# Kernel optimization log

Measured on AMD Instinct MI355X. Metric: run time of the kernel, lower is better.

Reference implementation:

```python
import jax, jax.numpy as jnp
import numpy as np

B, N, F_IN, H, F_OUT, NB = 4, 10000, 963, 128, 3, 3


def _gcn(x, adj, w, lw, b):
    # out = adj @ (x @ W) + x @ W_loop + bias   (adj shared across batch)
    return jnp.einsum('ij,bjf->bif', adj, x @ w) + x @ lw + b


def setup_inputs() -> dict:
    key = jax.random.key(0)
    ks = jax.random.split(key, 16)
    s = 0.02  # xavier-ish init scale
    adj = jax.random.uniform(ks[1], (N, N), dtype=jnp.float32) * (2.0 / N)  # normalized-adjacency surrogate
    return {
        'shape_verts': jax.random.normal(ks[0], (B, N, F_IN), dtype=jnp.float32),
        'adj': adj,
        'in_w': jax.random.normal(ks[2], (F_IN, H), dtype=jnp.float32) * s,
        'in_lw': jax.random.normal(ks[3], (F_IN, H), dtype=jnp.float32) * s,
        'in_b': jnp.zeros((H,), jnp.float32),
        'res_w1': jax.random.normal(ks[4], (NB, H, H), dtype=jnp.float32) * s,
        'res_lw1': jax.random.normal(ks[5], (NB, H, H), dtype=jnp.float32) * s,
        'res_b1': jnp.zeros((NB, H), jnp.float32),
        'res_w2': jax.random.normal(ks[6], (NB, H, H), dtype=jnp.float32) * s,
        'res_lw2': jax.random.normal(ks[7], (NB, H, H), dtype=jnp.float32) * s,
        'res_b2': jnp.zeros((NB, H), jnp.float32),
        'out_w': jax.random.normal(ks[8], (H, F_OUT), dtype=jnp.float32) * s,
        'out_lw': jax.random.normal(ks[9], (H, F_OUT), dtype=jnp.float32) * s,
        'out_b': jnp.zeros((F_OUT,), jnp.float32),
    }


def reference(shape_verts, adj, in_w, in_lw, in_b,
              res_w1, res_lw1, res_b1, res_w2, res_lw2, res_b2,
              out_w, out_lw, out_b):
    # GraphConvBottleneck.forward
    x = jax.nn.relu(_gcn(shape_verts, adj, in_w, in_lw, in_b))
    for i in range(NB):  # GraphConvResBlock
        h1 = jax.nn.relu(_gcn(x, adj, res_w1[i], res_lw1[i], res_b1[i]))
        h2 = jax.nn.relu(_gcn(h1, adj, res_w2[i], res_lw2[i], res_b2[i]))
        x = (x + h2) * 0.5
    x_out = _gcn(x, adj, out_w, out_lw, out_b)
    return (x_out, x)
```

## Files before the change

### kernel.cpp

```cpp
#include <hip/hip_runtime.h>
#include <stdint.h>

typedef unsigned short u16;
typedef __attribute__((ext_vector_type(8))) short short8;
typedef __attribute__((ext_vector_type(8))) unsigned short u16x8;
typedef __attribute__((ext_vector_type(4))) float f32x4;

#define NN    10000
#define NP    10016
#define MPADJ 10112
#define BB    4
#define HH    128
#define FIN   963
#define KIN   992
#define MR    40000
#define MRP   40064

__device__ __forceinline__ u16 f2bf(float f) {
  uint32_t u = __builtin_bit_cast(uint32_t, f);
  u += 0x7FFFu + ((u >> 16) & 1u);
  return (u16)(u >> 16);
}

__device__ __forceinline__ void gl2lds16(const void* g, void* l) {
  __builtin_amdgcn_global_load_lds((const __attribute__((address_space(1))) uint32_t*)g,
                                   (__attribute__((address_space(3))) uint32_t*)l, 16, 0, 0);
}


__global__ void conv_adj(const float* __restrict__ adj, u16* __restrict__ adjB) {
  int row = blockIdx.y;
  int j8 = blockIdx.x * 256 + threadIdx.x;
  if (j8 >= NP / 8) return;
  int j = j8 * 8;
  u16x8 o = {};
  if (row < NN && j < NN) {
    const float* p = adj + (size_t)row * NN + j;
    float4 a = *(const float4*)p;
    float4 b = *(const float4*)(p + 4);
    o[0] = f2bf(a.x); o[1] = f2bf(a.y); o[2] = f2bf(a.z); o[3] = f2bf(a.w);
    o[4] = f2bf(b.x); o[5] = f2bf(b.y); o[6] = f2bf(b.z); o[7] = f2bf(b.w);
  }
  *(u16x8*)(adjB + (size_t)row * NP + j) = o;
}

__global__ void conv_xin(const float* __restrict__ xin, u16* __restrict__ xinB) {
  int r = blockIdx.y;
  int f = blockIdx.x * 256 + threadIdx.x;
  if (f >= KIN) return;
  float v = 0.f;
  if (r < MR && f < FIN) v = xin[(size_t)r * FIN + f];
  xinB[(size_t)r * KIN + f] = f2bf(v);
}

__global__ void conv_w1(const float* __restrict__ wi, const float* __restrict__ lwi,
                        u16* __restrict__ Wt) {
  int tid = blockIdx.x * 256 + threadIdx.x;
  if (tid >= 256 * KIN) return;
  int c = tid / KIN, k = tid - c * KIN;
  float v = 0.f;
  if (k < FIN) v = (c < HH) ? wi[(size_t)k * HH + c] : lwi[(size_t)k * HH + (c - HH)];
  Wt[tid] = f2bf(v);
}

__global__ void conv_wres(const float* __restrict__ w1, const float* __restrict__ lw1,
                          const float* __restrict__ w2, const float* __restrict__ lw2,
                          u16* __restrict__ Wt) {
  int tid = blockIdx.x * 256 + threadIdx.x;
  if (tid >= 6 * 256 * HH) return;
  int l = tid / (256 * HH);
  int rem = tid - l * (256 * HH);
  int c = rem / HH, k = rem - c * HH;
  int blk = l >> 1;
  const float* W  = (l & 1) ? w2  : w1;
  const float* LW = (l & 1) ? lw2 : lw1;
  float v = (c < HH) ? W[((size_t)blk * HH + k) * HH + c]
                     : LW[((size_t)blk * HH + k) * HH + (c - HH)];
  Wt[tid] = f2bf(v);
}

__global__ void pad_zero(u16* tT, u16* xB, u16* h1B, u16* t3) {
  int tid = blockIdx.x * 256 + threadIdx.x;
  if (tid < 8192) {
    tT[(size_t)(tid >> 4) * NP + NN + (tid & 15)] = 0;
  } else if (tid < 16384) {
    xB[(size_t)MR * HH + (tid - 8192)] = 0;
  } else if (tid < 24576) {
    h1B[(size_t)MR * HH + (tid - 16384)] = 0;
  } else if (tid < 24832) {
    int t = tid - 24576;
    t3[(size_t)(t >> 4) * NP + NN + (t & 15)] = 0;
  }
}


__global__ __launch_bounds__(256) void gemm_big(const u16* __restrict__ A,
                                                const u16* __restrict__ Bt,
                                                float* __restrict__ P) {
  __shared__ u16 As[128 * 32];
  __shared__ u16 Bs[128 * 32];
  int mt_ = blockIdx.x, nt_ = blockIdx.y, s = blockIdx.z;
  int kt0 = (313 * s) / 3, kt1 = (313 * (s + 1)) / 3;
  int tid = threadIdx.x;
  int wave = tid >> 6, lane = tid & 63;
  int wm = wave >> 1, wn = wave & 1;
  int lr = lane >> 2, lc = (lane & 3) * 8;
  int ml = lane & 15, q = lane >> 4;

  const u16* Abase = A + (size_t)(mt_ * 128 + wave * 16 + lr) * NP + lc;
  const u16* Bbase = Bt + (size_t)(nt_ * 128 + wave * 16 + lr) * NP + lc;
  u16* lA = &As[(wave * 16) * 32];
  u16* lB = &Bs[(wave * 16) * 32];

  f32x4 acc[4][4] = {};
  for (int kt = kt0; kt < kt1; ++kt) {
    int k0 = kt * 32;
    __syncthreads();
    gl2lds16(Abase + k0, lA);
    gl2lds16(Abase + k0 + (size_t)64 * NP, lA + 64 * 32);
    gl2lds16(Bbase + k0, lB);
    gl2lds16(Bbase + k0 + (size_t)64 * NP, lB + 64 * 32);
    __syncthreads();
    short8 af[4], bf[4];
#pragma unroll
    for (int i = 0; i < 4; i++) af[i] = *(const short8*)&As[(wm * 64 + i * 16 + ml) * 32 + q * 8];
#pragma unroll
    for (int i = 0; i < 4; i++) bf[i] = *(const short8*)&Bs[(wn * 64 + i * 16 + ml) * 32 + q * 8];
#pragma unroll
    for (int i = 0; i < 4; i++)
#pragma unroll
      for (int j = 0; j < 4; j++)
        acc[i][j] = __builtin_amdgcn_mfma_f32_16x16x32_bf16(af[i], bf[j], acc[i][j], 0, 0, 0);
  }
  float* Ps = P + (size_t)s * NN * 512;
#pragma unroll
  for (int i = 0; i < 4; i++) {
    int row0 = mt_ * 128 + wm * 64 + i * 16 + q * 4;
#pragma unroll
    for (int j = 0; j < 4; j++) {
      int col = nt_ * 128 + wn * 64 + j * 16 + ml;
#pragma unroll
      for (int r = 0; r < 4; r++) {
        int row = row0 + r;
        if (row < NN) Ps[(size_t)row * 512 + col] = acc[i][j][r];
      }
    }
  }
}

__global__ __launch_bounds__(256) void gemm_small(const u16* __restrict__ A, int lda,
                                                  const u16* __restrict__ Wt, int ktiles,
                                                  const float* __restrict__ bias,
                                                  u16* __restrict__ tT, float* __restrict__ u) {
  __shared__ u16 As[128 * 32];
  __shared__ u16 Bs[128 * 32];
  int mt_ = blockIdx.x, half = blockIdx.y;
  int tid = threadIdx.x;
  int wave = tid >> 6, lane = tid & 63;
  int wm = wave >> 1, wn = wave & 1;
  int lr = lane >> 2, lc = (lane & 3) * 8;
  int ml = lane & 15, q = lane >> 4;

  const u16* Abase = A + (size_t)(mt_ * 128 + wave * 16 + lr) * lda + lc;
  const u16* Bbase = Wt + (size_t)(half * 128 + wave * 16 + lr) * lda + lc;
  u16* lA = &As[(wave * 16) * 32];
  u16* lB = &Bs[(wave * 16) * 32];

  f32x4 acc[4][4] = {};
  for (int kt = 0; kt < ktiles; ++kt) {
    int k0 = kt * 32;
    __syncthreads();
    gl2lds16(Abase + k0, lA);
    gl2lds16(Abase + k0 + (size_t)64 * lda, lA + 64 * 32);
    gl2lds16(Bbase + k0, lB);
    gl2lds16(Bbase + k0 + (size_t)64 * lda, lB + 64 * 32);
    __syncthreads();
    short8 af[4], bf[4];
#pragma unroll
    for (int i = 0; i < 4; i++) af[i] = *(const short8*)&As[(wm * 64 + i * 16 + ml) * 32 + q * 8];
#pragma unroll
    for (int i = 0; i < 4; i++) bf[i] = *(const short8*)&Bs[(wn * 64 + i * 16 + ml) * 32 + q * 8];
#pragma unroll
    for (int i = 0; i < 4; i++)
#pragma unroll
      for (int j = 0; j < 4; j++)
        acc[i][j] = __builtin_amdgcn_mfma_f32_16x16x32_bf16(af[i], bf[j], acc[i][j], 0, 0, 0);
  }
#pragma unroll
  for (int i = 0; i < 4; i++) {
    int row0 = mt_ * 128 + wm * 64 + i * 16 + q * 4;
#pragma unroll
    for (int j = 0; j < 4; j++) {
      int col = wn * 64 + j * 16 + ml;
#pragma unroll
      for (int r = 0; r < 4; r++) {
        int row = row0 + r;
        if (row < MR) {
          if (half == 0) {
            int b = row / NN;
            int n = row - b * NN;
            tT[(size_t)(b * 128 + col) * NP + n] = f2bf(acc[i][j][r]);
          } else {
            u[(size_t)row * HH + col] = acc[i][j][r] + bias[col];
          }
        }
      }
    }
  }
}

__global__ void reduce_act(const float* __restrict__ P, const float* __restrict__ u,
                           float* __restrict__ xf, u16* __restrict__ xB,
                           float* __restrict__ outx, int mode) {
  int tid = blockIdx.x * 256 + threadIdx.x;
  if (tid >= NN * 512) return;
  int n = tid >> 9, c = tid & 511;
  int b = c >> 7, h = c & 127;
  size_t uidx = (size_t)(b * NN + n) * HH + h;
  float v = P[tid] + P[5120000 + tid] + P[10240000 + tid] + u[uidx];
  v = v > 0.f ? v : 0.f;
  if (mode == 0) {
    xf[uidx] = v;
    xB[uidx] = f2bf(v);
  } else if (mode == 1) {
    xB[uidx] = f2bf(v);
  } else {
    float xn = (xf[uidx] + v) * 0.5f;
    xf[uidx] = xn;
    xB[uidx] = f2bf(xn);
    if (mode == 3) outx[uidx] = xn;
  }
}

__global__ void out_small(const float* __restrict__ x, const float* __restrict__ ow,
                          const float* __restrict__ olw, const float* __restrict__ ob,
                          u16* __restrict__ t3, float* __restrict__ u3) {
  int tid = blockIdx.x * 256 + threadIdx.x;
  if (tid >= NN * 16) return;
  int n = tid >> 4, c3 = tid & 15, b = c3 >> 2, f = c3 & 3;
  float tv = 0.f, uv = 0.f;
  if (f < 3) {
    const float* xr = x + (size_t)(b * NN + n) * HH;
    for (int k = 0; k < HH; k++) {
      float xv = xr[k];
      tv += xv * ow[k * 3 + f];
      uv += xv * olw[k * 3 + f];
    }
    uv += ob[f];
  }
  t3[(size_t)c3 * NP + n] = f2bf(tv);
  u3[tid] = uv;
}

__global__ __launch_bounds__(256) void gemm_skinny(const u16* __restrict__ A,
                                                   const u16* __restrict__ Bt,
                                                   float* __restrict__ P3) {
  __shared__ u16 As[64 * 32];
  __shared__ u16 Bs[16 * 32];
  int mt_ = blockIdx.x, s = blockIdx.y;
  int kt0 = (313 * s) / 2, kt1 = (313 * (s + 1)) / 2;
  int tid = threadIdx.x;
  int wave = tid >> 6, lane = tid & 63;
  int lr = lane >> 2, lc = (lane & 3) * 8;
  int ml = lane & 15, q = lane >> 4;

  const u16* Abase = A + (size_t)(mt_ * 64 + wave * 16 + lr) * NP + lc;
  const u16* Bbase = Bt + (size_t)lr * NP + lc;
  u16* lA = &As[(wave * 16) * 32];

  f32x4 acc = {};
  for (int kt = kt0; kt < kt1; ++kt) {
    int k0 = kt * 32;
    __syncthreads();
    gl2lds16(Abase + k0, lA);
    if (wave == 0) gl2lds16(Bbase + k0, &Bs[0]);
    __syncthreads();
    short8 af = *(const short8*)&As[(wave * 16 + ml) * 32 + q * 8];
    short8 bf = *(const short8*)&Bs[ml * 32 + q * 8];
    acc = __builtin_amdgcn_mfma_f32_16x16x32_bf16(af, bf, acc, 0, 0, 0);
  }
  float* Ps = P3 + (size_t)s * NP * 16;
  int row0 = mt_ * 64 + wave * 16 + q * 4;
#pragma unroll
  for (int r = 0; r < 4; r++) {
    int row = row0 + r;
    if (row < NN) Ps[(size_t)row * 16 + ml] = acc[r];
  }
}

__global__ void reduce3k(const float* __restrict__ P3, const float* __restrict__ u3,
                         float* __restrict__ out0) {
  int tid = blockIdx.x * 256 + threadIdx.x;
  if (tid >= NN * 12) return;
  int n = tid / 12;
  int rr = tid - n * 12;
  int b = rr / 3, f = rr - b * 3;
  int c3 = b * 4 + f;
  float v = P3[(size_t)n * 16 + c3] + P3[(size_t)NP * 16 + (size_t)n * 16 + c3] + u3[n * 16 + c3];
  out0[(size_t)(b * NN + n) * 3 + f] = v;
}


extern "C" void kernel_launch(void* const* d_in, const int* in_sizes, int n_in,
                              void* d_out, int out_size, void* d_ws, size_t ws_size,
                              hipStream_t stream) {
  (void)in_sizes; (void)n_in; (void)out_size; (void)ws_size;
  const float* xin    = (const float*)d_in[0];
  const float* adj    = (const float*)d_in[1];
  const float* in_w   = (const float*)d_in[2];
  const float* in_lw  = (const float*)d_in[3];
  const float* in_b   = (const float*)d_in[4];
  const float* res_w1 = (const float*)d_in[5];
  const float* res_lw1= (const float*)d_in[6];
  const float* res_b1 = (const float*)d_in[7];
  const float* res_w2 = (const float*)d_in[8];
  const float* res_lw2= (const float*)d_in[9];
  const float* res_b2 = (const float*)d_in[10];
  const float* out_w  = (const float*)d_in[11];
  const float* out_lw = (const float*)d_in[12];
  const float* out_b  = (const float*)d_in[13];

  char* wsp = (char*)d_ws;
  size_t off = 0;
  auto alloc = [&](size_t bytes) -> char* {
    char* p = wsp + off;
    off += (bytes + 255) & ~(size_t)255;
    return p;
  };
  u16*   adjB  = (u16*)alloc((size_t)MPADJ * NP * 2);
  char*  xinRg = alloc((size_t)MRP * KIN * 2);
  u16*   xinB  = (u16*)xinRg;
  float* P     = (float*)xinRg;
  u16*   WcatT = (u16*)alloc((size_t)256 * KIN * 2);
  u16*   WresT = (u16*)alloc((size_t)6 * 256 * HH * 2);
  u16*   tT    = (u16*)alloc((size_t)512 * NP * 2);
  float* u     = (float*)alloc((size_t)MR * HH * 4);
  float* xf    = (float*)alloc((size_t)MR * HH * 4);
  u16*   xB    = (u16*)alloc((size_t)MRP * HH * 2);
  u16*   h1B   = (u16*)alloc((size_t)MRP * HH * 2);
  u16*   t3    = (u16*)alloc((size_t)16 * NP * 2);
  float* u3    = (float*)alloc((size_t)NN * 16 * 4);
  float* P3    = (float*)alloc((size_t)2 * NP * 16 * 4);

  float* out0 = (float*)d_out;
  float* out1 = (float*)d_out + (size_t)BB * NN * 3;

  {
    dim3 g((NP / 8 + 255) / 256, MPADJ);
    conv_adj<<<g, 256, 0, stream>>>(adj, adjB);
  }
  {
    dim3 g((KIN + 255) / 256, MRP);
    conv_xin<<<g, 256, 0, stream>>>(xin, xinB);
  }
  conv_w1<<<(256 * KIN + 255) / 256, 256, 0, stream>>>(in_w, in_lw, WcatT);
  conv_wres<<<(6 * 256 * HH + 255) / 256, 256, 0, stream>>>(res_w1, res_lw1, res_w2, res_lw2, WresT);
  pad_zero<<<(24832 + 255) / 256, 256, 0, stream>>>(tT, xB, h1B, t3);

  dim3 gsmall(313, 2);
  dim3 gbig(79, 4, 3);
  int nred = (NN * 512 + 255) / 256;

  gemm_small<<<gsmall, 256, 0, stream>>>(xinB, KIN, WcatT, KIN / 32, in_b, tT, u);
  gemm_big<<<gbig, 256, 0, stream>>>(adjB, tT, P);
  reduce_act<<<nred, 256, 0, stream>>>(P, u, xf, xB, nullptr, 0);

  for (int blk = 0; blk < 3; blk++) {
    gemm_small<<<gsmall, 256, 0, stream>>>(xB, HH, WresT + (size_t)(2 * blk) * 256 * HH,
                                           HH / 32, res_b1 + blk * HH, tT, u);
    gemm_big<<<gbig, 256, 0, stream>>>(adjB, tT, P);
    reduce_act<<<nred, 256, 0, stream>>>(P, u, nullptr, h1B, nullptr, 1);

    gemm_small<<<gsmall, 256, 0, stream>>>(h1B, HH, WresT + (size_t)(2 * blk + 1) * 256 * HH,
                                           HH / 32, res_b2 + blk * HH, tT, u);
    gemm_big<<<gbig, 256, 0, stream>>>(adjB, tT, P);
    reduce_act<<<nred, 256, 0, stream>>>(P, u, xf, xB, out1, (blk == 2) ? 3 : 2);
  }

  out_small<<<(NN * 16 + 255) / 256, 256, 0, stream>>>(xf, out_w, out_lw, out_b, t3, u3);
  {
    dim3 g(157, 2);
    gemm_skinny<<<g, 256, 0, stream>>>(adjB, t3, P3);
  }
  reduce3k<<<(NN * 12 + 255) / 256, 256, 0, stream>>>(P3, u3, out0);
}
```

Baseline: 2.615 ms.

## Pre-tile adjacency and t operands into contiguous 128x32 bf16 blocks for GEMMs

Stores the bf16 adjacency and the transposed t operands in a tiled layout where each 128x32 (or 16x32) K-tile is contiguous, so each wave's global-to-LDS loads read a single contiguous 1 KB run. gemm_big now uses 512-thread blocks covering a 128x256 output tile, which halves how often the adjacency is re-read across N tiles. gemm_skinny moves to 128-row tiles with a 4-way K split and reduce3k sums four partials. The cost is extra index arithmetic in the producers, scattered 2-byte writes to tT, and higher register pressure under launch_bounds(512,4).

```diff
diff --git a/kernel.cpp b/kernel.cpp
--- a/kernel.cpp
+++ b/kernel.cpp
@@ -8,6 +8,7 @@
 
 #define NN    10000
 #define NP    10016
+#define NKT   313
 #define MPADJ 10112
 #define BB    4
 #define HH    128
@@ -28,20 +29,26 @@
 }
 
 
-__global__ void conv_adj(const float* __restrict__ adj, u16* __restrict__ adjB) {
-  int row = blockIdx.y;
-  int j8 = blockIdx.x * 256 + threadIdx.x;
-  if (j8 >= NP / 8) return;
-  int j = j8 * 8;
-  u16x8 o = {};
-  if (row < NN && j < NN) {
-    const float* p = adj + (size_t)row * NN + j;
+__global__ void conv_adj(const float* __restrict__ adj, u16* __restrict__ adjP) {
+  int mt = blockIdx.x, kt = blockIdx.y;
+  int t = threadIdx.x;
+  int tr = t >> 1, ch = (t & 1) * 16;
+  int row = mt * 128 + tr, col = kt * 32 + ch;
+  u16x8 o0 = {}, o1 = {};
+  if (row < NN && col < NN) {
+    const float* p = adj + (size_t)row * NN + col;
     float4 a = *(const float4*)p;
     float4 b = *(const float4*)(p + 4);
-    o[0] = f2bf(a.x); o[1] = f2bf(a.y); o[2] = f2bf(a.z); o[3] = f2bf(a.w);
-    o[4] = f2bf(b.x); o[5] = f2bf(b.y); o[6] = f2bf(b.z); o[7] = f2bf(b.w);
-  }
-  *(u16x8*)(adjB + (size_t)row * NP + j) = o;
+    float4 c = *(const float4*)(p + 8);
+    float4 d = *(const float4*)(p + 12);
+    o0[0] = f2bf(a.x); o0[1] = f2bf(a.y); o0[2] = f2bf(a.z); o0[3] = f2bf(a.w);
+    o0[4] = f2bf(b.x); o0[5] = f2bf(b.y); o0[6] = f2bf(b.z); o0[7] = f2bf(b.w);
+    o1[0] = f2bf(c.x); o1[1] = f2bf(c.y); o1[2] = f2bf(c.z); o1[3] = f2bf(c.w);
+    o1[4] = f2bf(d.x); o1[5] = f2bf(d.y); o1[6] = f2bf(d.z); o1[7] = f2bf(d.w);
+  }
+  u16* dst = adjP + ((size_t)mt * NKT + kt) * 4096 + tr * 32 + ch;
+  *(u16x8*)dst = o0;
+  *(u16x8*)(dst + 8) = o1;
 }
 
 __global__ void conv_xin(const float* __restrict__ xin, u16* __restrict__ xinB) {
@@ -82,50 +89,54 @@
 __global__ void pad_zero(u16* tT, u16* xB, u16* h1B, u16* t3) {
   int tid = blockIdx.x * 256 + threadIdx.x;
   if (tid < 8192) {
-    tT[(size_t)(tid >> 4) * NP + NN + (tid & 15)] = 0;
+    int b = tid >> 11, rem = tid & 2047;
+    int h = rem >> 4, k = rem & 15;
+    tT[((size_t)(b * NKT + 312) * 128 + h) * 32 + 16 + k] = 0;
   } else if (tid < 16384) {
     xB[(size_t)MR * HH + (tid - 8192)] = 0;
   } else if (tid < 24576) {
     h1B[(size_t)MR * HH + (tid - 16384)] = 0;
   } else if (tid < 24832) {
     int t = tid - 24576;
-    t3[(size_t)(t >> 4) * NP + NN + (t & 15)] = 0;
-  }
-}
-
-
-__global__ __launch_bounds__(256) void gemm_big(const u16* __restrict__ A,
-                                                const u16* __restrict__ Bt,
-                                                float* __restrict__ P) {
+    int c3 = t >> 4, k = t & 15;
+    t3[(size_t)(312 * 16 + c3) * 32 + 16 + k] = 0;
+  }
+}
+
+
+__global__ __launch_bounds__(512, 4) void gemm_big(const u16* __restrict__ A,
+                                                   const u16* __restrict__ Bt,
+                                                   float* __restrict__ P) {
   __shared__ u16 As[128 * 32];
-  __shared__ u16 Bs[128 * 32];
-  int mt_ = blockIdx.x, nt_ = blockIdx.y, s = blockIdx.z;
-  int kt0 = (313 * s) / 3, kt1 = (313 * (s + 1)) / 3;
+  __shared__ u16 Bs[256 * 32];
+  int mt = blockIdx.x, ntb = blockIdx.y, s = blockIdx.z;
+  int kt0 = (NKT * s) / 3, kt1 = (NKT * (s + 1)) / 3;
   int tid = threadIdx.x;
-  int wave = tid >> 6, lane = tid & 63;
-  int wm = wave >> 1, wn = wave & 1;
-  int lr = lane >> 2, lc = (lane & 3) * 8;
+  int w = tid >> 6, lane = tid & 63;
+  int wm = w >> 2, wn = w & 3;
   int ml = lane & 15, q = lane >> 4;
 
-  const u16* Abase = A + (size_t)(mt_ * 128 + wave * 16 + lr) * NP + lc;
-  const u16* Bbase = Bt + (size_t)(nt_ * 128 + wave * 16 + lr) * NP + lc;
-  u16* lA = &As[(wave * 16) * 32];
-  u16* lB = &Bs[(wave * 16) * 32];
+  const u16* pa = A + ((size_t)mt * NKT + kt0) * 4096 + w * 512 + lane * 8;
+  int seg0 = w * 2, seg1 = w * 2 + 1;
+  const u16* pb0 = Bt + ((size_t)(ntb * 2 + (seg0 >> 3)) * NKT + kt0) * 4096 + (seg0 & 7) * 512 + lane * 8;
+  const u16* pb1 = Bt + ((size_t)(ntb * 2 + (seg1 >> 3)) * NKT + kt0) * 4096 + (seg1 & 7) * 512 + lane * 8;
+  u16* lA  = As + w * 512;
+  u16* lB0 = Bs + seg0 * 512;
+  u16* lB1 = Bs + seg1 * 512;
 
   f32x4 acc[4][4] = {};
   for (int kt = kt0; kt < kt1; ++kt) {
-    int k0 = kt * 32;
-    __syncthreads();
-    gl2lds16(Abase + k0, lA);
-    gl2lds16(Abase + k0 + (size_t)64 * NP, lA + 64 * 32);
-    gl2lds16(Bbase + k0, lB);
-    gl2lds16(Bbase + k0 + (size_t)64 * NP, lB + 64 * 32);
+    __syncthreads();
+    gl2lds16(pa, lA);
+    gl2lds16(pb0, lB0);
+    gl2lds16(pb1, lB1);
+    pa += 4096; pb0 += 4096; pb1 += 4096;
     __syncthreads();
     short8 af[4], bf[4];
 #pragma unroll
     for (int i = 0; i < 4; i++) af[i] = *(const short8*)&As[(wm * 64 + i * 16 + ml) * 32 + q * 8];
 #pragma unroll
-    for (int i = 0; i < 4; i++) bf[i] = *(const short8*)&Bs[(wn * 64 + i * 16 + ml) * 32 + q * 8];
+    for (int j = 0; j < 4; j++) bf[j] = *(const short8*)&Bs[(wn * 64 + j * 16 + ml) * 32 + q * 8];
 #pragma unroll
     for (int i = 0; i < 4; i++)
 #pragma unroll
@@ -135,10 +146,10 @@
   float* Ps = P + (size_t)s * NN * 512;
 #pragma unroll
   for (int i = 0; i < 4; i++) {
-    int row0 = mt_ * 128 + wm * 64 + i * 16 + q * 4;
+    int row0 = mt * 128 + wm * 64 + i * 16 + q * 4;
 #pragma unroll
     for (int j = 0; j < 4; j++) {
-      int col = nt_ * 128 + wn * 64 + j * 16 + ml;
+      int col = ntb * 256 + wn * 64 + j * 16 + ml;
 #pragma unroll
       for (int r = 0; r < 4; r++) {
         int row = row0 + r;
@@ -199,7 +210,7 @@
           if (half == 0) {
             int b = row / NN;
             int n = row - b * NN;
-            tT[(size_t)(b * 128 + col) * NP + n] = f2bf(acc[i][j][r]);
+            tT[((size_t)(b * NKT + (n >> 5)) * 128 + col) * 32 + (n & 31)] = f2bf(acc[i][j][r]);
           } else {
             u[(size_t)row * HH + col] = acc[i][j][r] + bias[col];
           }
@@ -248,43 +259,50 @@
     }
     uv += ob[f];
   }
-  t3[(size_t)c3 * NP + n] = f2bf(tv);
+  t3[((size_t)(n >> 5) * 16 + c3) * 32 + (n & 31)] = f2bf(tv);
   u3[tid] = uv;
 }
 
 __global__ __launch_bounds__(256) void gemm_skinny(const u16* __restrict__ A,
                                                    const u16* __restrict__ Bt,
                                                    float* __restrict__ P3) {
-  __shared__ u16 As[64 * 32];
+  __shared__ u16 As[128 * 32];
   __shared__ u16 Bs[16 * 32];
-  int mt_ = blockIdx.x, s = blockIdx.y;
-  int kt0 = (313 * s) / 2, kt1 = (313 * (s + 1)) / 2;
+  int mt = blockIdx.x, s = blockIdx.y;
+  int kt0 = (NKT * s) / 4, kt1 = (NKT * (s + 1)) / 4;
   int tid = threadIdx.x;
-  int wave = tid >> 6, lane = tid & 63;
-  int lr = lane >> 2, lc = (lane & 3) * 8;
+  int w = tid >> 6, lane = tid & 63;
   int ml = lane & 15, q = lane >> 4;
 
-  const u16* Abase = A + (size_t)(mt_ * 64 + wave * 16 + lr) * NP + lc;
-  const u16* Bbase = Bt + (size_t)lr * NP + lc;
-  u16* lA = &As[(wave * 16) * 32];
-
-  f32x4 acc = {};
+  const u16* pa = A + ((size_t)mt * NKT + kt0) * 4096 + w * 512 + lane * 8;
+  const u16* pb = Bt + (size_t)kt0 * 512 + lane * 8;
+  u16* lA0 = As + w * 512;
+  u16* lA1 = As + 2048 + w * 512;
+
+  f32x4 acc[2] = {};
   for (int kt = kt0; kt < kt1; ++kt) {
-    int k0 = kt * 32;
-    __syncthreads();
-    gl2lds16(Abase + k0, lA);
-    if (wave == 0) gl2lds16(Bbase + k0, &Bs[0]);
-    __syncthreads();
-    short8 af = *(const short8*)&As[(wave * 16 + ml) * 32 + q * 8];
+    __syncthreads();
+    gl2lds16(pa, lA0);
+    gl2lds16(pa + 2048, lA1);
+    if (w == 0) gl2lds16(pb, Bs);
+    pa += 4096; pb += 512;
+    __syncthreads();
     short8 bf = *(const short8*)&Bs[ml * 32 + q * 8];
-    acc = __builtin_amdgcn_mfma_f32_16x16x32_bf16(af, bf, acc, 0, 0, 0);
+#pragma unroll
+    for (int i = 0; i < 2; i++) {
+      short8 af = *(const short8*)&As[(w * 32 + i * 16 + ml) * 32 + q * 8];
+      acc[i] = __builtin_amdgcn_mfma_f32_16x16x32_bf16(af, bf, acc[i], 0, 0, 0);
+    }
   }
   float* Ps = P3 + (size_t)s * NP * 16;
-  int row0 = mt_ * 64 + wave * 16 + q * 4;
-#pragma unroll
-  for (int r = 0; r < 4; r++) {
-    int row = row0 + r;
-    if (row < NN) Ps[(size_t)row * 16 + ml] = acc[r];
+#pragma unroll
+  for (int i = 0; i < 2; i++) {
+    int row0 = mt * 128 + w * 32 + i * 16 + q * 4;
+#pragma unroll
+    for (int r = 0; r < 4; r++) {
+      int row = row0 + r;
+      if (row < NN) Ps[(size_t)row * 16 + ml] = acc[i][r];
+    }
   }
 }
 
@@ -296,7 +314,10 @@
   int rr = tid - n * 12;
   int b = rr / 3, f = rr - b * 3;
   int c3 = b * 4 + f;
-  float v = P3[(size_t)n * 16 + c3] + P3[(size_t)NP * 16 + (size_t)n * 16 + c3] + u3[n * 16 + c3];
+  size_t stride = (size_t)NP * 16;
+  float v = P3[(size_t)n * 16 + c3] + P3[stride + n * 16 + c3]
+          + P3[2 * stride + n * 16 + c3] + P3[3 * stride + n * 16 + c3]
+          + u3[n * 16 + c3];
   out0[(size_t)(b * NN + n) * 3 + f] = v;
 }
 
@@ -327,26 +348,26 @@
     off += (bytes + 255) & ~(size_t)255;
     return p;
   };
-  u16*   adjB  = (u16*)alloc((size_t)MPADJ * NP * 2);
+  u16*   adjB  = (u16*)alloc((size_t)79 * NKT * 4096 * 2);
   char*  xinRg = alloc((size_t)MRP * KIN * 2);
   u16*   xinB  = (u16*)xinRg;
   float* P     = (float*)xinRg;
   u16*   WcatT = (u16*)alloc((size_t)256 * KIN * 2);
   u16*   WresT = (u16*)alloc((size_t)6 * 256 * HH * 2);
-  u16*   tT    = (u16*)alloc((size_t)512 * NP * 2);
+  u16*   tT    = (u16*)alloc((size_t)4 * NKT * 4096 * 2);
   float* u     = (float*)alloc((size_t)MR * HH * 4);
   float* xf    = (float*)alloc((size_t)MR * HH * 4);
   u16*   xB    = (u16*)alloc((size_t)MRP * HH * 2);
   u16*   h1B   = (u16*)alloc((size_t)MRP * HH * 2);
-  u16*   t3    = (u16*)alloc((size_t)16 * NP * 2);
+  u16*   t3    = (u16*)alloc((size_t)NKT * 16 * 32 * 2);
   float* u3    = (float*)alloc((size_t)NN * 16 * 4);
-  float* P3    = (float*)alloc((size_t)2 * NP * 16 * 4);
+  float* P3    = (float*)alloc((size_t)4 * NP * 16 * 4);
 
   float* out0 = (float*)d_out;
   float* out1 = (float*)d_out + (size_t)BB * NN * 3;
 
   {
-    dim3 g((NP / 8 + 255) / 256, MPADJ);
+    dim3 g(79, NKT);
     conv_adj<<<g, 256, 0, stream>>>(adj, adjB);
   }
   {
@@ -358,28 +379,28 @@
   pad_zero<<<(24832 + 255) / 256, 256, 0, stream>>>(tT, xB, h1B, t3);
 
   dim3 gsmall(313, 2);
-  dim3 gbig(79, 4, 3);
+  dim3 gbig(79, 2, 3);
   int nred = (NN * 512 + 255) / 256;
 
   gemm_small<<<gsmall, 256, 0, stream>>>(xinB, KIN, WcatT, KIN / 32, in_b, tT, u);
-  gemm_big<<<gbig, 256, 0, stream>>>(adjB, tT, P);
+  gemm_big<<<gbig, 512, 0, stream>>>(adjB, tT, P);
   reduce_act<<<nred, 256, 0, stream>>>(P, u, xf, xB, nullptr, 0);
 
   for (int blk = 0; blk < 3; blk++) {
     gemm_small<<<gsmall, 256, 0, stream>>>(xB, HH, WresT + (size_t)(2 * blk) * 256 * HH,
                                            HH / 32, res_b1 + blk * HH, tT, u);
-    gemm_big<<<gbig, 256, 0, stream>>>(adjB, tT, P);
+    gemm_big<<<gbig, 512, 0, stream>>>(adjB, tT, P);
     reduce_act<<<nred, 256, 0, stream>>>(P, u, nullptr, h1B, nullptr, 1);
 
     gemm_small<<<gsmall, 256, 0, stream>>>(h1B, HH, WresT + (size_t)(2 * blk + 1) * 256 * HH,
                                            HH / 32, res_b2 + blk * HH, tT, u);
-    gemm_big<<<gbig, 256, 0, stream>>>(adjB, tT, P);
+    gemm_big<<<gbig, 512, 0, stream>>>(adjB, tT, P);
     reduce_act<<<nred, 256, 0, stream>>>(P, u, xf, xB, out1, (blk == 2) ? 3 : 2);
   }
 
   out_small<<<(NN * 16 + 255) / 256, 256, 0, stream>>>(xf, out_w, out_lw, out_b, t3, u3);
   {
-    dim3 g(157, 2);
+    dim3 g(79, 4);
     gemm_skinny<<<g, 256, 0, stream>>>(adjB, t3, P3);
   }
   reduce3k<<<(NN * 12 + 255) / 256, 256, 0, stream>>>(P3, u3, out0);
```

After: 2.124 ms. -18.8%, faster.
